# Kernel tuning notes

Hardware: AMD Instinct MI355X
Metric: run time of the kernel (lower is better)

Reference implementation:

```python
import jax, jax.numpy as jnp
import numpy as np

N_NODES = 50000
N_EDGES = 1600000
IN_FEATS = 128
ENC_H = 20
DEC_H = 64


def setup_inputs() -> dict:
    key = jax.random.key(0)
    ks = jax.random.split(key, 14)
    inp = {}
    inp["x"] = jax.random.normal(ks[0], (N_NODES, IN_FEATS), dtype=jnp.float32)
    inp["edge_index"] = jax.random.randint(ks[1], (2, N_EDGES), 0, N_NODES, dtype=jnp.int64)
    inp["node_id"] = 0
    inp["noise_normal"] = jax.random.normal(ks[2], (N_EDGES, ENC_H), dtype=jnp.float32)
    inp["noise_u"] = jax.random.uniform(ks[3], (N_EDGES, 1), dtype=jnp.float32)
    # parameters (glorot-ish init)
    def lin(k, fan_in, fan_out):
        s = 1.0 / np.sqrt(fan_in)
        return jax.random.uniform(k, (fan_in, fan_out), jnp.float32, -s, s)
    inp["W_gc"] = lin(ks[4], IN_FEATS, ENC_H)
    inp["b_gc"] = jnp.zeros((ENC_H,), jnp.float32)
    inp["W_mu"] = lin(ks[5], 3 * ENC_H, ENC_H)
    inp["b_mu"] = jnp.zeros((ENC_H,), jnp.float32)
    inp["W_var"] = lin(ks[6], 3 * ENC_H, ENC_H)
    inp["b_var"] = jnp.zeros((ENC_H,), jnp.float32)
    inp["W_d1"] = lin(ks[7], ENC_H, DEC_H)
    inp["b_d1"] = jnp.zeros((DEC_H,), jnp.float32)
    inp["W_d2"] = lin(ks[8], DEC_H, 1)
    inp["b_d2"] = jnp.zeros((1,), jnp.float32)
    return inp


def _gcn_conv(x, edge_index, W, b):
    """PyG-style GCNConv: add self-loops, symmetric D^-1/2 (A+I) D^-1/2 norm."""
    n = x.shape[0]
    sl = jnp.arange(n, dtype=edge_index.dtype)
    row = jnp.concatenate([edge_index[0], sl])  # source
    col = jnp.concatenate([edge_index[1], sl])  # target
    xw = x @ W  # [N, H]
    deg = jax.ops.segment_sum(jnp.ones_like(col, dtype=xw.dtype), col, num_segments=n)
    dinv = jnp.where(deg > 0, jax.lax.rsqrt(deg), 0.0)
    norm = dinv[row] * dinv[col]  # [E+N]
    out = jax.ops.segment_sum(xw[row] * norm[:, None], col, num_segments=n)
    return out + b


def reference(x, edge_index, node_id, noise_normal, noise_u,
              W_gc, b_gc, W_mu, b_mu, W_var, b_var, W_d1, b_d1, W_d2, b_d2):
    # GCN encoder
    x1 = jax.nn.relu(_gcn_conv(x, edge_index, W_gc, b_gc))  # [N, H]
    # per-edge concat: [src_embed | dst_embed | node_id_embed]
    rows, cols = edge_index[0], edge_index[1]
    node_embed = jnp.broadcast_to(x1[node_id][None, :], (rows.shape[0], x1.shape[1]))
    x2 = jnp.concatenate([x1[rows], x1[cols], node_embed], axis=1)  # [E, 3H]
    # variational heads + reparameterization
    mu = x2 @ W_mu + b_mu
    sigma = jnp.exp(x2 @ W_var + b_var)
    z = mu + sigma * noise_normal  # [E, H]
    # decoder MLP
    h = jax.nn.relu(z @ W_d1 + b_d1)
    sampling_weights = jax.nn.relu(h @ W_d2 + b_d2)  # [E, 1]
    # gumbel-sigmoid sample (training=True, bias=0.0 -> bias'=1e-4, temperature=1.0)
    bias = 0.0001
    eps = (bias - (1.0 - bias)) * noise_u + (1.0 - bias)
    gate = jnp.log(eps) - jnp.log(1.0 - eps) + sampling_weights
    return jax.nn.sigmoid(gate)
```

## Files before the change

kernel.cpp:

```cpp
#include <hip/hip_runtime.h>

#define NFEAT 128
#define H 20
#define DH 64
#define SCAN_T 1024
#define BE 64
#define NB 192
#define HW 12800

typedef __attribute__((ext_vector_type(8))) short short8;
typedef __attribute__((ext_vector_type(4))) float f32x4;

__device__ __forceinline__ unsigned short f2bf(float f) {
    union { float f; unsigned u; } v; v.f = f;
    unsigned r = v.u + 0x7fff + ((v.u >> 16) & 1);
    return (unsigned short)(r >> 16);
}
__device__ __forceinline__ unsigned pk2(unsigned short a, unsigned short b) {
    return (unsigned)a | ((unsigned)b << 16);
}

template <int CTRL>
__device__ __forceinline__ float dpp_add(float x) {
    int y = __builtin_amdgcn_update_dpp(0, __float_as_int(x), CTRL, 0xF, 0xF, true);
    return x + __int_as_float(y);
}
__device__ __forceinline__ float sum16(float x) {
    x = dpp_add<0xB1>(x);
    x = dpp_add<0x4E>(x);
    x = dpp_add<0x124>(x);
    x = dpp_add<0x128>(x);
    return x;
}

__global__ __launch_bounds__(256) void k_prep(const float* __restrict__ Wmu, const float* __restrict__ Wvar,
                                              const float* __restrict__ Wd1,
                                              unsigned short* __restrict__ Bh, unsigned short* __restrict__ Bd1,
                                              int* __restrict__ deg, int* __restrict__ csum, int N) {
    int t = blockIdx.x * blockDim.x + threadIdx.x;
    if (t < N) deg[t] = 0;
    if (t < 256) csum[t] = 0;
    if (t < 512) {
        int f = t >> 6, l = t & 63;
        int tile = f >> 1, s = f & 1;
        int col = (tile & 1) * 16 + (l & 15);
        const float* W = (tile < 2) ? Wmu : Wvar;
#pragma unroll
        for (int j = 0; j < 8; j++) {
            int k = s * 32 + (l >> 4) * 8 + j;
            float v = (k < 2 * H && col < H) ? W[k * H + col] : 0.f;
            Bh[(size_t)f * 512 + l * 8 + j] = f2bf(v);
        }
    } else if (t < 768) {
        int f = (t - 512) >> 6, l = t & 63;
        int n = f * 16 + (l & 15);
#pragma unroll
        for (int j = 0; j < 8; j++) {
            int k = (l >> 4) * 8 + j;
            float v = (k < H) ? Wd1[k * DH + n] : 0.f;
            Bd1[(size_t)f * 512 + l * 8 + j] = f2bf(v);
        }
    }
}

__global__ __launch_bounds__(512) void k_hist(const int* __restrict__ cols,
                                              unsigned* __restrict__ hist, int* __restrict__ csum,
                                              int E, int N) {
    __shared__ unsigned h[HW];
    __shared__ int cs[256];
    int wstride = (N + 3) >> 2;
    int nchunks = (N + 255) >> 8;
    for (int i = threadIdx.x; i < wstride; i += 512) h[i] = 0;
    if (threadIdx.x < 256) cs[threadIdx.x] = 0;
    __syncthreads();
    int chunk = (E + NB - 1) / NB;
    int beg = blockIdx.x * chunk, end = min(beg + chunk, E);
    for (int i = beg + threadIdx.x; i < end; i += 512) {
        int c = __builtin_nontemporal_load(cols + i);
        atomicAdd(&h[c >> 2], 1u << ((c & 3) * 8));
    }
    __syncthreads();
    unsigned* dst = hist + (size_t)blockIdx.x * wstride;
    for (int i = threadIdx.x; i < wstride; i += 512) {
        unsigned w = h[i];
        dst[i] = w;
        if (w) {
            int s = (w & 0xFF) + ((w >> 8) & 0xFF) + ((w >> 16) & 0xFF) + (w >> 24);
            atomicAdd(&cs[i >> 6], s);
        }
    }
    __syncthreads();
    for (int j = threadIdx.x; j < nchunks; j += 512)
        if (cs[j]) atomicAdd(&csum[j], cs[j]);
}

__global__ __launch_bounds__(256) void k_scansmall(const int* __restrict__ chunkSum,
                                                   int* __restrict__ chunkOff, int nb) {
    __shared__ int sc[256];
    int t = threadIdx.x;
    int v0 = (t < nb) ? chunkSum[t] : 0;
    sc[t] = v0;
    __syncthreads();
    for (int off = 1; off < 256; off <<= 1) {
        int v = (t >= off) ? sc[t - off] : 0;
        __syncthreads();
        sc[t] += v;
        __syncthreads();
    }
    if (t < nb) chunkOff[t] = sc[t] - v0;
}

__global__ __launch_bounds__(256) void k_bases(const unsigned* __restrict__ hist,
                                               const int* __restrict__ chunkOff,
                                               unsigned char* __restrict__ delta,
                                               int* __restrict__ offsets, int* __restrict__ deg,
                                               int N, int E) {
    __shared__ int sc[256];
    int c = blockIdx.x * 256 + threadIdx.x;
    int wstride = (N + 3) >> 2;
    int sh = (c & 3) * 8;
    bool valid = c < N;
    int cw = valid ? (c >> 2) : 0;
    unsigned cnt[NB / 4];
    int d = 0;
#pragma unroll
    for (int b = 0; b < NB; b++) {
        unsigned w = hist[(size_t)b * wstride + cw];
        unsigned byte = (w >> sh) & 0xFF;
        if ((b & 3) == 0) cnt[b >> 2] = byte;
        else cnt[b >> 2] |= byte << ((b & 3) * 8);
        d += (int)byte;
    }
    if (!valid) d = 0;
    sc[threadIdx.x] = d;
    __syncthreads();
    for (int off = 1; off < 256; off <<= 1) {
        int v = (threadIdx.x >= off) ? sc[threadIdx.x - off] : 0;
        __syncthreads();
        sc[threadIdx.x] += v;
        __syncthreads();
    }
    if (valid) {
        int base = chunkOff[blockIdx.x] + sc[threadIdx.x] - d;
        offsets[c] = base;
        deg[c] = d;
        int run = 0;
#pragma unroll
        for (int b = 0; b < NB; b++) {
            delta[(size_t)b * N + c] = (unsigned char)run;
            run += (int)((cnt[b >> 2] >> ((b & 3) * 8)) & 0xFF);
        }
    }
    if (blockIdx.x == 0 && threadIdx.x == 0) offsets[N] = E;
}

__global__ __launch_bounds__(512) void k_place(const int* __restrict__ rows, const int* __restrict__ cols,
                                               const int* __restrict__ offsets,
                                               const unsigned char* __restrict__ delta,
                                               unsigned short* __restrict__ srcs, int E, int N) {
    __shared__ unsigned h[HW];
    int wstride = (N + 3) >> 2;
    for (int i = threadIdx.x; i < wstride; i += 512) h[i] = 0;
    __syncthreads();
    int chunk = (E + NB - 1) / NB;
    int beg = blockIdx.x * chunk, end = min(beg + chunk, E);
    const unsigned char* mydelta = delta + (size_t)blockIdx.x * N;
    for (int i = beg + threadIdx.x; i < end; i += 512) {
        int c = __builtin_nontemporal_load(cols + i);
        int r = __builtin_nontemporal_load(rows + i);
        int sh = (c & 3) * 8;
        unsigned old = atomicAdd(&h[c >> 2], 1u << sh);
        int rank = (old >> sh) & 0xFF;
        int pos = offsets[c] + (int)mydelta[c] + rank;
        srcs[pos] = (unsigned short)r;
    }
}

__global__ __launch_bounds__(256) void k_deg(const int* __restrict__ cols, int* __restrict__ deg, int E) {
    int t = blockIdx.x * blockDim.x + threadIdx.x;
    if (t < E) atomicAdd(&deg[cols[t]], 1);
}

__global__ __launch_bounds__(SCAN_T) void k_scan(const int* __restrict__ deg, int* __restrict__ offsets,
                                                 int* __restrict__ cursor, int N) {
    __shared__ int sums[SCAN_T];
    int t = threadIdx.x;
    int chunk = (N + SCAN_T - 1) / SCAN_T;
    int beg = t * chunk;
    int end = min(beg + chunk, N);
    int s = 0;
    for (int i = beg; i < end; i++) s += deg[i];
    sums[t] = s;
    __syncthreads();
    for (int off = 1; off < SCAN_T; off <<= 1) {
        int v = (t >= off) ? sums[t - off] : 0;
        __syncthreads();
        sums[t] += v;
        __syncthreads();
    }
    int run = (t == 0) ? 0 : sums[t - 1];
    for (int i = beg; i < end; i++) {
        offsets[i] = run;
        cursor[i] = run;
        run += deg[i];
    }
    if (t == SCAN_T - 1) offsets[N] = sums[SCAN_T - 1];
}

__global__ __launch_bounds__(256) void k_bucket_csr(const int* __restrict__ rows, const int* __restrict__ cols,
                                                    int* __restrict__ cursor, int* __restrict__ srcs, int E) {
    int e = blockIdx.x * blockDim.x + threadIdx.x;
    if (e >= E) return;
    int pos = atomicAdd(&cursor[cols[e]], 1);
    srcs[pos] = rows[e];
}

__global__ __launch_bounds__(256) void k_xw_xs(const float* __restrict__ x, const float* __restrict__ Wgc,
                                               const int* __restrict__ deg,
                                               float* __restrict__ xs, int N) {
    __shared__ float Ws[NFEAT * H];
    for (int i = threadIdx.x; i < NFEAT * H; i += blockDim.x) Ws[i] = Wgc[i];
    __syncthreads();
    int n = blockIdx.x * blockDim.x + threadIdx.x;
    if (n >= N) return;
    float acc[H];
#pragma unroll
    for (int j = 0; j < H; j++) acc[j] = 0.f;
    const float4* x4 = (const float4*)(x + (size_t)n * NFEAT);
#pragma unroll 4
    for (int k4 = 0; k4 < NFEAT / 4; k4++) {
        float4 xv = x4[k4];
#pragma unroll
        for (int s = 0; s < 4; s++) {
            float xk = (s == 0) ? xv.x : (s == 1) ? xv.y : (s == 2) ? xv.z : xv.w;
            const float4* wrow = (const float4*)(Ws + (k4 * 4 + s) * H);
#pragma unroll
            for (int q = 0; q < 5; q++) {
                float4 w = wrow[q];
                acc[q * 4 + 0] += xk * w.x;
                acc[q * 4 + 1] += xk * w.y;
                acc[q * 4 + 2] += xk * w.z;
                acc[q * 4 + 3] += xk * w.w;
            }
        }
    }
    float di = rsqrtf((float)(deg[n] + 1));
    float4* o = (float4*)(xs + (size_t)n * H);
#pragma unroll
    for (int q = 0; q < 5; q++)
        o[q] = make_float4(acc[q * 4 + 0] * di, acc[q * 4 + 1] * di, acc[q * 4 + 2] * di, acc[q * 4 + 3] * di);
}

template <typename IT>
__device__ __forceinline__ void gather_core16(const float* __restrict__ xs, const IT* __restrict__ idx,
                                              int beg, int end, int n, int sl, int degn,
                                              const float* __restrict__ bgc, unsigned short* __restrict__ x1b,
                                              int nid, const float* __restrict__ Wmu, const float* __restrict__ Wvar,
                                              const float* __restrict__ bmu, const float* __restrict__ bvar,
                                              float* __restrict__ bcat2) {
    float acc[H];
    if (sl == 0) {
        const float4* self = (const float4*)(xs + (size_t)n * H);
#pragma unroll
        for (int q = 0; q < 5; q++) {
            float4 v = self[q];
            acc[q * 4 + 0] = v.x; acc[q * 4 + 1] = v.y; acc[q * 4 + 2] = v.z; acc[q * 4 + 3] = v.w;
        }
    } else {
#pragma unroll
        for (int j = 0; j < H; j++) acc[j] = 0.f;
    }
#pragma unroll 2
    for (int i = beg + sl; i < end; i += 16) {
        int r = (int)__builtin_nontemporal_load(idx + i);
        const float4* p = (const float4*)(xs + (size_t)r * H);
#pragma unroll
        for (int q = 0; q < 5; q++) {
            float4 v = p[q];
            acc[q * 4 + 0] += v.x; acc[q * 4 + 1] += v.y; acc[q * 4 + 2] += v.z; acc[q * 4 + 3] += v.w;
        }
    }
#pragma unroll
    for (int j = 0; j < H; j++) acc[j] = sum16(acc[j]);
    float di = rsqrtf((float)(degn + 1));
    float x1f[H];
#pragma unroll
    for (int j = 0; j < H; j++) x1f[j] = fmaxf(di * acc[j] + bgc[j], 0.f);
    if (sl == 0) {
        unsigned o[10];
#pragma unroll
        for (int j = 0; j < 10; j++) o[j] = pk2(f2bf(x1f[2 * j]), f2bf(x1f[2 * j + 1]));
        unsigned* dst = (unsigned*)(x1b + (size_t)n * H);
        *(uint4*)dst = make_uint4(o[0], o[1], o[2], o[3]);
        *(uint4*)(dst + 4) = make_uint4(o[4], o[5], o[6], o[7]);
        *(uint2*)(dst + 8) = make_uint2(o[8], o[9]);
    }
    if (n == nid) {
#pragma unroll
        for (int base = 0; base < 48; base += 16) {
            int jj = base + sl;
            if (jj < 40) {
                bool ismu = jj < 20;
                int col = ismu ? jj : jj - 20;
                const float* W = ismu ? Wmu : Wvar;
                float s = ismu ? bmu[col] : bvar[col];
#pragma unroll
                for (int k = 0; k < H; k++) s += x1f[k] * W[(2 * H + k) * H + col];
                bcat2[jj] = s;
            }
        }
    }
}

__global__ __launch_bounds__(256) void k_gather_csr16(const float* __restrict__ xs, const unsigned short* __restrict__ srcs,
                                                      const int* __restrict__ offsets, const int* __restrict__ deg,
                                                      const float* __restrict__ bgc,
                                                      unsigned short* __restrict__ x1b,
                                                      const int* __restrict__ node_id,
                                                      const float* __restrict__ Wmu, const float* __restrict__ Wvar,
                                                      const float* __restrict__ bmu, const float* __restrict__ bvar,
                                                      float* __restrict__ bcat2, int N) {
    int wave = (blockIdx.x * 256 + threadIdx.x) >> 6;
    int lane = threadIdx.x & 63;
    int n = wave * 4 + (lane >> 4);
    if (n >= N) return;
    gather_core16(xs, srcs, offsets[n], offsets[n + 1], n, lane & 15, deg[n], bgc, x1b,
                  node_id[0], Wmu, Wvar, bmu, bvar, bcat2);
}

__global__ __launch_bounds__(256) void k_gather_csr(const float* __restrict__ xs, const int* __restrict__ srcs,
                                                    const int* __restrict__ offsets, const int* __restrict__ deg,
                                                    const float* __restrict__ bgc,
                                                    unsigned short* __restrict__ x1b,
                                                    const int* __restrict__ node_id,
                                                    const float* __restrict__ Wmu, const float* __restrict__ Wvar,
                                                    const float* __restrict__ bmu, const float* __restrict__ bvar,
                                                    float* __restrict__ bcat2, int N) {
    int wave = (blockIdx.x * 256 + threadIdx.x) >> 6;
    int lane = threadIdx.x & 63;
    int n = wave * 4 + (lane >> 4);
    if (n >= N) return;
    gather_core16(xs, srcs, offsets[n], offsets[n + 1], n, lane & 15, deg[n], bgc, x1b,
                  node_id[0], Wmu, Wvar, bmu, bvar, bcat2);
}

__global__ __launch_bounds__(256, 8) void k_mlp(
    const unsigned short* __restrict__ x1b, const int* __restrict__ rows, const int* __restrict__ cols,
    const float* __restrict__ noise_n, const float* __restrict__ noise_u,
    const unsigned short* __restrict__ Bh, const unsigned short* __restrict__ Bd1g,
    const float* __restrict__ bcat2, const float* __restrict__ b_d1,
    const float* __restrict__ W_d2, const float* __restrict__ b_d2,
    float* __restrict__ out, int E) {

    __shared__ __align__(16) unsigned short x2s[BE * 72];
    __shared__ __align__(16) unsigned short A2[BE * 44];

    int tid = threadIdx.x;
    int e0 = blockIdx.x * BE;
    int l = tid & 63, w = tid >> 6;
    int m = l & 15, quad = l >> 4;
    int erow0 = w * 16 + quad * 4;

    float nz0[4], nz1[4];
#pragma unroll
    for (int r4 = 0; r4 < 4; r4++) {
        int e = e0 + erow0 + r4;
        int ec = (e < E) ? e : 0;
        nz0[r4] = noise_n[(size_t)ec * H + m];
        nz1[r4] = (m < 4) ? noise_n[(size_t)ec * H + 16 + m] : 0.f;
    }

    {
        int le = tid >> 2, p = tid & 3;
        int e = e0 + le; if (e >= E) e = E - 1;
        int r = rows[e], c = cols[e];
#pragma unroll
        for (int ii = 0; ii < 4; ii++) {
            int i = p + ii * 4;
            unsigned* dst = (unsigned*)((char*)x2s + le * 144 + i * 8);
            if (i < 10) {
                int node = (i < 5) ? r : c;
                int cc = (i < 5) ? i : i - 5;
                uint2 v = *(const uint2*)((const char*)x1b + (size_t)node * 40 + cc * 8);
                dst[0] = v.x;
                dst[1] = v.y;
            } else {
                dst[0] = 0u; dst[1] = 0u;
            }
        }
    }
    __syncthreads();

    f32x4 accs[4];
    {
        const char* arow = (const char*)x2s + (w * 16 + m) * 144 + quad * 16;
        short8 a0 = *(const short8*)(arow);
        short8 a1 = *(const short8*)(arow + 64);
#pragma unroll
        for (int t4 = 0; t4 < 4; t4++) {
            f32x4 acc = {0.f, 0.f, 0.f, 0.f};
            short8 b0 = *(const short8*)(Bh + (t4 * 2 + 0) * 512 + l * 8);
            short8 b1 = *(const short8*)(Bh + (t4 * 2 + 1) * 512 + l * 8);
            acc = __builtin_amdgcn_mfma_f32_16x16x32_bf16(a0, b0, acc, 0, 0, 0);
            acc = __builtin_amdgcn_mfma_f32_16x16x32_bf16(a1, b1, acc, 0, 0, 0);
            accs[t4] = acc;
        }
    }

    {
        float bm0 = bcat2[m];
        float bv0 = bcat2[20 + m];
        float bm1 = (m < 4) ? bcat2[16 + m] : 0.f;
        float bv1 = (m < 4) ? bcat2[36 + m] : 0.f;
#pragma unroll
        for (int r4 = 0; r4 < 4; r4++) {
            float z0 = accs[0][r4] + bm0 + __expf(accs[2][r4] + bv0) * nz0[r4];
            *(unsigned short*)((char*)A2 + (erow0 + r4) * 88 + m * 2) = f2bf(z0);
            unsigned short z1v = 0;
            if (m < 4) z1v = f2bf(accs[1][r4] + bm1 + __expf(accs[3][r4] + bv1) * nz1[r4]);
            *(unsigned short*)((char*)A2 + (erow0 + r4) * 88 + (16 + m) * 2) = z1v;
        }
    }
    __syncthreads();

    {
        short8 a2 = *(const short8*)((const char*)A2 + (w * 16 + m) * 88 + quad * 16);
        float p0 = 0.f, p1 = 0.f, p2 = 0.f, p3 = 0.f;
#pragma unroll
        for (int t4 = 0; t4 < 4; t4++) {
            f32x4 acc = {0.f, 0.f, 0.f, 0.f};
            short8 bb = *(const short8*)(Bd1g + t4 * 512 + l * 8);
            acc = __builtin_amdgcn_mfma_f32_16x16x32_bf16(a2, bb, acc, 0, 0, 0);
            int col = t4 * 16 + m;
            float bias = b_d1[col], wo = W_d2[col];
            p0 += fmaxf(acc[0] + bias, 0.f) * wo;
            p1 += fmaxf(acc[1] + bias, 0.f) * wo;
            p2 += fmaxf(acc[2] + bias, 0.f) * wo;
            p3 += fmaxf(acc[3] + bias, 0.f) * wo;
        }
        p0 = sum16(p0); p1 = sum16(p1); p2 = sum16(p2); p3 = sum16(p3);
        if (m < 4) {
            float swv = (m == 0) ? p0 : (m == 1) ? p1 : (m == 2) ? p2 : p3;
            int leo = w * 16 + quad * 4 + m;
            int e = e0 + leo;
            if (e < E) {
                float sw = fmaxf(swv + b_d2[0], 0.f);
                float u = noise_u[e];
                float ev = 0.9999f - 0.9998f * u;
                float t = __expf(-sw);
                out[e] = ev / (ev + (1.f - ev) * t);
            }
        }
    }
}

extern "C" void kernel_launch(void* const* d_in, const int* in_sizes, int n_in,
                              void* d_out, int out_size, void* d_ws, size_t ws_size,
                              hipStream_t stream) {
    const int N = in_sizes[0] / NFEAT;
    const int E = in_sizes[1] / 2;

    const float* x       = (const float*)d_in[0];
    const int*   ei      = (const int*)d_in[1];
    const int*   rows    = ei;
    const int*   cols    = ei + E;
    const int*   node_id = (const int*)d_in[2];
    const float* noise_n = (const float*)d_in[3];
    const float* noise_u = (const float*)d_in[4];
    const float* Wgc  = (const float*)d_in[5];
    const float* bgc  = (const float*)d_in[6];
    const float* Wmu  = (const float*)d_in[7];
    const float* bmu  = (const float*)d_in[8];
    const float* Wvar = (const float*)d_in[9];
    const float* bvar = (const float*)d_in[10];
    const float* Wd1  = (const float*)d_in[11];
    const float* bd1  = (const float*)d_in[12];
    const float* Wd2  = (const float*)d_in[13];
    const float* bd2  = (const float*)d_in[14];
    float* out = (float*)d_out;

    const int B = 256;
    int gN  = (N + B - 1) / B;
    int gG  = (N + 15) / 16;
    int gE  = (E + B - 1) / B;
    int gM  = (E + BE - 1) / BE;
    int nBins = (N + 255) / 256;

    char* ws = (char*)d_ws;
    size_t o_deg     = 0;
    size_t o_off     = o_deg  + (((size_t)N * 4 + 255) & ~255ULL);
    size_t o_csum    = o_off  + (((size_t)(N + 1) * 4 + 255) & ~255ULL);
    size_t o_coff    = o_csum + 1024;
    size_t o_hist    = o_coff + 1024;
    size_t wstride   = (size_t)((N + 3) >> 2);
    size_t o_delta   = o_hist  + ((NB * wstride * 4 + 255) & ~255ULL);
    size_t o_srcs    = o_delta + (((size_t)NB * N + 255) & ~255ULL);
    size_t o_xs      = o_srcs  + (((size_t)E * 2 + 255) & ~255ULL);
    size_t o_x1b     = o_xs    + (((size_t)N * H * 4 + 255) & ~255ULL);
    size_t o_Bh      = o_x1b   + (((size_t)N * H * 2 + 255) & ~255ULL);
    size_t o_Bd1     = o_Bh    + 8192;
    size_t o_bcat2   = o_Bd1   + 4096;
    size_t need      = o_bcat2 + 256;

    bool main_path = (ws_size >= need) && (N <= 4 * HW) && (N < 65536) && (nBins <= 256);

    if (main_path) {
        int*   deg     = (int*)(ws + o_deg);
        int*   offsets = (int*)(ws + o_off);
        int*   csum    = (int*)(ws + o_csum);
        int*   coff    = (int*)(ws + o_coff);
        unsigned* hist = (unsigned*)(ws + o_hist);
        unsigned char* delta = (unsigned char*)(ws + o_delta);
        unsigned short* srcs = (unsigned short*)(ws + o_srcs);
        float* xs      = (float*)(ws + o_xs);
        unsigned short* x1b  = (unsigned short*)(ws + o_x1b);
        unsigned short* Bh   = (unsigned short*)(ws + o_Bh);
        unsigned short* Bd1  = (unsigned short*)(ws + o_Bd1);
        float* bcat2   = (float*)(ws + o_bcat2);

        k_prep<<<gN, B, 0, stream>>>(Wmu, Wvar, Wd1, Bh, Bd1, deg, csum, N);
        k_hist<<<NB, 512, 0, stream>>>(cols, hist, csum, E, N);
        k_scansmall<<<1, B, 0, stream>>>(csum, coff, nBins);
        k_bases<<<nBins, B, 0, stream>>>(hist, coff, delta, offsets, deg, N, E);
        k_xw_xs<<<gN, B, 0, stream>>>(x, Wgc, deg, xs, N);
        k_place<<<NB, 512, 0, stream>>>(rows, cols, offsets, delta, srcs, E, N);
        k_gather_csr16<<<gG, B, 0, stream>>>(xs, srcs, offsets, deg, bgc, x1b,
                                             node_id, Wmu, Wvar, bmu, bvar, bcat2, N);
        k_mlp<<<gM, B, 0, stream>>>(x1b, rows, cols, noise_n, noise_u,
                                    Bh, Bd1, bcat2, bd1, Wd2, bd2, out, E);
    } else {
        int*   deg     = (int*)ws;
        int*   offsets = (int*)(ws + 200000);
        int*   cursor  = (int*)(ws + 400016);
        int*   srcs    = (int*)(ws + 600016);
        float* xs      = (float*)(ws + 7000016);
        unsigned short* x1b = (unsigned short*)(ws + 11000016);
        unsigned short* Bh  = (unsigned short*)(ws + 13000016);
        unsigned short* Bd1 = (unsigned short*)(ws + 13008208);
        float* bcat2   = (float*)(ws + 13012304);

        k_prep<<<gN, B, 0, stream>>>(Wmu, Wvar, Wd1, Bh, Bd1, deg, cursor, N);
        k_deg<<<gE, B, 0, stream>>>(cols, deg, E);
        k_scan<<<1, SCAN_T, 0, stream>>>(deg, offsets, cursor, N);
        k_bucket_csr<<<gE, B, 0, stream>>>(rows, cols, cursor, srcs, E);
        k_xw_xs<<<gN, B, 0, stream>>>(x, Wgc, deg, xs, N);
        k_gather_csr<<<gG, B, 0, stream>>>(xs, srcs, offsets, deg, bgc, x1b,
                                           node_id, Wmu, Wvar, bmu, bvar, bcat2, N);
        k_mlp<<<gM, B, 0, stream>>>(x1b, rows, cols, noise_n, noise_u,
                                    Bh, Bd1, bcat2, bd1, Wd2, bd2, out, E);
    }
}
```

Before: 430.4 us.

## Precompute per-node mu/var projections and drop per-edge head GEMM

Because x2 is a concatenation, the mu and var heads split into a per-source term, a per-destination term and a constant node_id term. The gather kernel now computes the per-node projections x1·W_mu and x1·W_var for the source and destination weight blocks and stores them in bf16 as PA and PB. The edge MLP then only gathers two 96-byte rows and adds them, which removes the shared-memory staging, a barrier and the first MFMA stage per edge. The cost is more per-node work and a larger per-node table, which reuses the histogram workspace region. bcat2 is also zeroed in prep, in case the node_id term is never written.

```diff
diff --git a/kernel.cpp b/kernel.cpp
--- a/kernel.cpp
+++ b/kernel.cpp
@@ -19,6 +19,11 @@
 __device__ __forceinline__ unsigned pk2(unsigned short a, unsigned short b) {
     return (unsigned)a | ((unsigned)b << 16);
 }
+__device__ __forceinline__ float bfel(uint4 v, int j) {
+    unsigned word = (j < 2) ? v.x : (j < 4) ? v.y : (j < 6) ? v.z : v.w;
+    unsigned u = (j & 1) ? (word & 0xFFFF0000u) : (word << 16);
+    return __int_as_float((int)u);
+}
 
 template <int CTRL>
 __device__ __forceinline__ float dpp_add(float x) {
@@ -33,26 +38,16 @@
     return x;
 }
 
-__global__ __launch_bounds__(256) void k_prep(const float* __restrict__ Wmu, const float* __restrict__ Wvar,
-                                              const float* __restrict__ Wd1,
-                                              unsigned short* __restrict__ Bh, unsigned short* __restrict__ Bd1,
-                                              int* __restrict__ deg, int* __restrict__ csum, int N) {
+__global__ __launch_bounds__(256) void k_prep(const float* __restrict__ Wd1,
+                                              unsigned short* __restrict__ Bd1,
+                                              int* __restrict__ deg, int* __restrict__ csum,
+                                              float* __restrict__ bcat2, int N) {
     int t = blockIdx.x * blockDim.x + threadIdx.x;
     if (t < N) deg[t] = 0;
     if (t < 256) csum[t] = 0;
-    if (t < 512) {
+    if (t < 64) bcat2[t] = 0.f;
+    if (t < 256) {
         int f = t >> 6, l = t & 63;
-        int tile = f >> 1, s = f & 1;
-        int col = (tile & 1) * 16 + (l & 15);
-        const float* W = (tile < 2) ? Wmu : Wvar;
-#pragma unroll
-        for (int j = 0; j < 8; j++) {
-            int k = s * 32 + (l >> 4) * 8 + j;
-            float v = (k < 2 * H && col < H) ? W[k * H + col] : 0.f;
-            Bh[(size_t)f * 512 + l * 8 + j] = f2bf(v);
-        }
-    } else if (t < 768) {
-        int f = (t - 512) >> 6, l = t & 63;
         int n = f * 16 + (l & 15);
 #pragma unroll
         for (int j = 0; j < 8; j++) {
@@ -254,7 +249,8 @@
 template <typename IT>
 __device__ __forceinline__ void gather_core16(const float* __restrict__ xs, const IT* __restrict__ idx,
                                               int beg, int end, int n, int sl, int degn,
-                                              const float* __restrict__ bgc, unsigned short* __restrict__ x1b,
+                                              const float* __restrict__ bgc,
+                                              unsigned short* __restrict__ PAo, unsigned short* __restrict__ PBo,
                                               int nid, const float* __restrict__ Wmu, const float* __restrict__ Wvar,
                                               const float* __restrict__ bmu, const float* __restrict__ bvar,
                                               float* __restrict__ bcat2) {
@@ -286,15 +282,24 @@
     float x1f[H];
 #pragma unroll
     for (int j = 0; j < H; j++) x1f[j] = fmaxf(di * acc[j] + bgc[j], 0.f);
-    if (sl == 0) {
-        unsigned o[10];
-#pragma unroll
-        for (int j = 0; j < 10; j++) o[j] = pk2(f2bf(x1f[2 * j]), f2bf(x1f[2 * j + 1]));
-        unsigned* dst = (unsigned*)(x1b + (size_t)n * H);
-        *(uint4*)dst = make_uint4(o[0], o[1], o[2], o[3]);
-        *(uint4*)(dst + 4) = make_uint4(o[4], o[5], o[6], o[7]);
-        *(uint2*)(dst + 8) = make_uint2(o[8], o[9]);
-    }
+
+#pragma unroll
+    for (int t = 0; t < 6; t++) {
+        int v = sl + 16 * t;
+        int part = v / 24;
+        int j = v - part * 24;
+        float s = 0.f;
+        if (j < 20) {
+            const float* W = (part & 1) ? Wvar : Wmu;
+            int k0 = (part < 2) ? 0 : 20;
+#pragma unroll
+            for (int k = 0; k < H; k++) s += x1f[k] * W[(k0 + k) * H + j];
+        }
+        unsigned short* T = (part < 2) ? PAo : PBo;
+        int off = (j >> 3) * 16 + (part & 1) * 8 + (j & 7);
+        T[(size_t)n * 48 + off] = f2bf(s);
+    }
+
     if (n == nid) {
 #pragma unroll
         for (int base = 0; base < 48; base += 16) {
@@ -315,7 +320,7 @@
 __global__ __launch_bounds__(256) void k_gather_csr16(const float* __restrict__ xs, const unsigned short* __restrict__ srcs,
                                                       const int* __restrict__ offsets, const int* __restrict__ deg,
                                                       const float* __restrict__ bgc,
-                                                      unsigned short* __restrict__ x1b,
+                                                      unsigned short* __restrict__ PAo, unsigned short* __restrict__ PBo,
                                                       const int* __restrict__ node_id,
                                                       const float* __restrict__ Wmu, const float* __restrict__ Wvar,
                                                       const float* __restrict__ bmu, const float* __restrict__ bvar,
@@ -324,14 +329,14 @@
     int lane = threadIdx.x & 63;
     int n = wave * 4 + (lane >> 4);
     if (n >= N) return;
-    gather_core16(xs, srcs, offsets[n], offsets[n + 1], n, lane & 15, deg[n], bgc, x1b,
+    gather_core16(xs, srcs, offsets[n], offsets[n + 1], n, lane & 15, deg[n], bgc, PAo, PBo,
                   node_id[0], Wmu, Wvar, bmu, bvar, bcat2);
 }
 
 __global__ __launch_bounds__(256) void k_gather_csr(const float* __restrict__ xs, const int* __restrict__ srcs,
                                                     const int* __restrict__ offsets, const int* __restrict__ deg,
                                                     const float* __restrict__ bgc,
-                                                    unsigned short* __restrict__ x1b,
+                                                    unsigned short* __restrict__ PAo, unsigned short* __restrict__ PBo,
                                                     const int* __restrict__ node_id,
                                                     const float* __restrict__ Wmu, const float* __restrict__ Wvar,
                                                     const float* __restrict__ bmu, const float* __restrict__ bvar,
@@ -340,116 +345,96 @@
     int lane = threadIdx.x & 63;
     int n = wave * 4 + (lane >> 4);
     if (n >= N) return;
-    gather_core16(xs, srcs, offsets[n], offsets[n + 1], n, lane & 15, deg[n], bgc, x1b,
+    gather_core16(xs, srcs, offsets[n], offsets[n + 1], n, lane & 15, deg[n], bgc, PAo, PBo,
                   node_id[0], Wmu, Wvar, bmu, bvar, bcat2);
 }
 
-__global__ __launch_bounds__(256, 8) void k_mlp(
-    const unsigned short* __restrict__ x1b, const int* __restrict__ rows, const int* __restrict__ cols,
+__global__ __launch_bounds__(256) void k_mlp(
+    const unsigned short* __restrict__ PA, const unsigned short* __restrict__ PBt,
+    const int* __restrict__ rows, const int* __restrict__ cols,
     const float* __restrict__ noise_n, const float* __restrict__ noise_u,
-    const unsigned short* __restrict__ Bh, const unsigned short* __restrict__ Bd1g,
+    const unsigned short* __restrict__ Bd1g,
     const float* __restrict__ bcat2, const float* __restrict__ b_d1,
     const float* __restrict__ W_d2, const float* __restrict__ b_d2,
     float* __restrict__ out, int E) {
-
-    __shared__ __align__(16) unsigned short x2s[BE * 72];
-    __shared__ __align__(16) unsigned short A2[BE * 44];
 
     int tid = threadIdx.x;
     int e0 = blockIdx.x * BE;
     int l = tid & 63, w = tid >> 6;
     int m = l & 15, quad = l >> 4;
-    int erow0 = w * 16 + quad * 4;
-
-    float nz0[4], nz1[4];
-#pragma unroll
-    for (int r4 = 0; r4 < 4; r4++) {
-        int e = e0 + erow0 + r4;
-        int ec = (e < E) ? e : 0;
-        nz0[r4] = noise_n[(size_t)ec * H + m];
-        nz1[r4] = (m < 4) ? noise_n[(size_t)ec * H + 16 + m] : 0.f;
-    }
-
-    {
-        int le = tid >> 2, p = tid & 3;
-        int e = e0 + le; if (e >= E) e = E - 1;
-        int r = rows[e], c = cols[e];
-#pragma unroll
-        for (int ii = 0; ii < 4; ii++) {
-            int i = p + ii * 4;
-            unsigned* dst = (unsigned*)((char*)x2s + le * 144 + i * 8);
-            if (i < 10) {
-                int node = (i < 5) ? r : c;
-                int cc = (i < 5) ? i : i - 5;
-                uint2 v = *(const uint2*)((const char*)x1b + (size_t)node * 40 + cc * 8);
-                dst[0] = v.x;
-                dst[1] = v.y;
-            } else {
-                dst[0] = 0u; dst[1] = 0u;
-            }
-        }
-    }
-    __syncthreads();
-
-    f32x4 accs[4];
-    {
-        const char* arow = (const char*)x2s + (w * 16 + m) * 144 + quad * 16;
-        short8 a0 = *(const short8*)(arow);
-        short8 a1 = *(const short8*)(arow + 64);
-#pragma unroll
-        for (int t4 = 0; t4 < 4; t4++) {
-            f32x4 acc = {0.f, 0.f, 0.f, 0.f};
-            short8 b0 = *(const short8*)(Bh + (t4 * 2 + 0) * 512 + l * 8);
-            short8 b1 = *(const short8*)(Bh + (t4 * 2 + 1) * 512 + l * 8);
-            acc = __builtin_amdgcn_mfma_f32_16x16x32_bf16(a0, b0, acc, 0, 0, 0);
-            acc = __builtin_amdgcn_mfma_f32_16x16x32_bf16(a1, b1, acc, 0, 0, 0);
-            accs[t4] = acc;
-        }
-    }
-
-    {
-        float bm0 = bcat2[m];
-        float bv0 = bcat2[20 + m];
-        float bm1 = (m < 4) ? bcat2[16 + m] : 0.f;
-        float bv1 = (m < 4) ? bcat2[36 + m] : 0.f;
-#pragma unroll
-        for (int r4 = 0; r4 < 4; r4++) {
-            float z0 = accs[0][r4] + bm0 + __expf(accs[2][r4] + bv0) * nz0[r4];
-            *(unsigned short*)((char*)A2 + (erow0 + r4) * 88 + m * 2) = f2bf(z0);
-            unsigned short z1v = 0;
-            if (m < 4) z1v = f2bf(accs[1][r4] + bm1 + __expf(accs[3][r4] + bv1) * nz1[r4]);
-            *(unsigned short*)((char*)A2 + (erow0 + r4) * 88 + (16 + m) * 2) = z1v;
-        }
-    }
-    __syncthreads();
-
-    {
-        short8 a2 = *(const short8*)((const char*)A2 + (w * 16 + m) * 88 + quad * 16);
-        float p0 = 0.f, p1 = 0.f, p2 = 0.f, p3 = 0.f;
-#pragma unroll
-        for (int t4 = 0; t4 < 4; t4++) {
-            f32x4 acc = {0.f, 0.f, 0.f, 0.f};
-            short8 bb = *(const short8*)(Bd1g + t4 * 512 + l * 8);
-            acc = __builtin_amdgcn_mfma_f32_16x16x32_bf16(a2, bb, acc, 0, 0, 0);
-            int col = t4 * 16 + m;
-            float bias = b_d1[col], wo = W_d2[col];
-            p0 += fmaxf(acc[0] + bias, 0.f) * wo;
-            p1 += fmaxf(acc[1] + bias, 0.f) * wo;
-            p2 += fmaxf(acc[2] + bias, 0.f) * wo;
-            p3 += fmaxf(acc[3] + bias, 0.f) * wo;
-        }
-        p0 = sum16(p0); p1 = sum16(p1); p2 = sum16(p2); p3 = sum16(p3);
-        if (m < 4) {
-            float swv = (m == 0) ? p0 : (m == 1) ? p1 : (m == 2) ? p2 : p3;
-            int leo = w * 16 + quad * 4 + m;
-            int e = e0 + leo;
-            if (e < E) {
-                float sw = fmaxf(swv + b_d2[0], 0.f);
-                float u = noise_u[e];
-                float ev = 0.9999f - 0.9998f * u;
-                float t = __expf(-sw);
-                out[e] = ev / (ev + (1.f - ev) * t);
-            }
+
+    int ea = e0 + w * 16 + m;
+    int ec = (ea < E) ? ea : E - 1;
+    int r = rows[ec], c = cols[ec];
+
+    uint4 pam = {0, 0, 0, 0}, pav = {0, 0, 0, 0}, pbm = {0, 0, 0, 0}, pbv = {0, 0, 0, 0};
+    float nz[8], bm[8], bv[8];
+#pragma unroll
+    for (int j = 0; j < 8; j++) { nz[j] = 0.f; bm[j] = 0.f; bv[j] = 0.f; }
+    if (quad < 3) {
+        const char* pa = (const char*)PA + (size_t)r * 96 + quad * 32;
+        const char* pb = (const char*)PBt + (size_t)c * 96 + quad * 32;
+        pam = *(const uint4*)pa;  pav = *(const uint4*)(pa + 16);
+        pbm = *(const uint4*)pb;  pbv = *(const uint4*)(pb + 16);
+        float4 b0 = *(const float4*)(bcat2 + quad * 8);
+        float4 b1 = *(const float4*)(bcat2 + quad * 8 + 4);
+        bm[0] = b0.x; bm[1] = b0.y; bm[2] = b0.z; bm[3] = b0.w;
+        bm[4] = b1.x; bm[5] = b1.y; bm[6] = b1.z; bm[7] = b1.w;
+        float4 v0 = *(const float4*)(bcat2 + 20 + quad * 8);
+        float4 v1 = *(const float4*)(bcat2 + 20 + quad * 8 + 4);
+        bv[0] = v0.x; bv[1] = v0.y; bv[2] = v0.z; bv[3] = v0.w;
+        bv[4] = v1.x; bv[5] = v1.y; bv[6] = v1.z; bv[7] = v1.w;
+        const float* np = noise_n + (size_t)ec * H + quad * 8;
+        float4 n0 = *(const float4*)np;
+        nz[0] = n0.x; nz[1] = n0.y; nz[2] = n0.z; nz[3] = n0.w;
+        if (quad < 2) {
+            float4 n1 = *(const float4*)(np + 4);
+            nz[4] = n1.x; nz[5] = n1.y; nz[6] = n1.z; nz[7] = n1.w;
+        }
+    }
+
+    unsigned zp[4];
+#pragma unroll
+    for (int jj = 0; jj < 4; jj++) {
+        unsigned short zh[2];
+#pragma unroll
+        for (int h2 = 0; h2 < 2; h2++) {
+            int j = jj * 2 + h2;
+            float zmu = bfel(pam, j) + bfel(pbm, j) + bm[j];
+            float zva = bfel(pav, j) + bfel(pbv, j) + bv[j];
+            float z = zmu + __expf(zva) * nz[j];
+            z = (quad * 8 + j < 20) ? z : 0.f;
+            zh[h2] = f2bf(z);
+        }
+        zp[jj] = pk2(zh[0], zh[1]);
+    }
+    union { unsigned u[4]; short8 s; } au;
+    au.u[0] = zp[0]; au.u[1] = zp[1]; au.u[2] = zp[2]; au.u[3] = zp[3];
+    short8 a2 = au.s;
+
+    float p0 = 0.f, p1 = 0.f, p2 = 0.f, p3 = 0.f;
+#pragma unroll
+    for (int t4 = 0; t4 < 4; t4++) {
+        f32x4 acc = {0.f, 0.f, 0.f, 0.f};
+        short8 bb = *(const short8*)(Bd1g + t4 * 512 + l * 8);
+        acc = __builtin_amdgcn_mfma_f32_16x16x32_bf16(a2, bb, acc, 0, 0, 0);
+        int col = t4 * 16 + m;
+        float bias = b_d1[col], wo = W_d2[col];
+        p0 += fmaxf(acc[0] + bias, 0.f) * wo;
+        p1 += fmaxf(acc[1] + bias, 0.f) * wo;
+        p2 += fmaxf(acc[2] + bias, 0.f) * wo;
+        p3 += fmaxf(acc[3] + bias, 0.f) * wo;
+    }
+    p0 = sum16(p0); p1 = sum16(p1); p2 = sum16(p2); p3 = sum16(p3);
+    if (m < 4) {
+        float swv = (m == 0) ? p0 : (m == 1) ? p1 : (m == 2) ? p2 : p3;
+        int e = e0 + w * 16 + quad * 4 + m;
+        if (e < E) {
+            float sw = fmaxf(swv + b_d2[0], 0.f);
+            float u = noise_u[e];
+            float ev = 0.9999f - 0.9998f * u;
+            float t = __expf(-sw);
+            out[e] = ev / (ev + (1.f - ev) * t);
         }
     }
 }
@@ -487,18 +472,19 @@
     int nBins = (N + 255) / 256;
 
     char* ws = (char*)d_ws;
+    size_t wstride   = (size_t)((N + 3) >> 2);
+    size_t pa_sz     = (((size_t)N * 96) + 255) & ~255ULL;
+    size_t hist_sz   = ((NB * wstride * 4) + 255) & ~255ULL;
+    size_t histreg   = (hist_sz > 2 * pa_sz) ? hist_sz : 2 * pa_sz;
     size_t o_deg     = 0;
     size_t o_off     = o_deg  + (((size_t)N * 4 + 255) & ~255ULL);
     size_t o_csum    = o_off  + (((size_t)(N + 1) * 4 + 255) & ~255ULL);
     size_t o_coff    = o_csum + 1024;
     size_t o_hist    = o_coff + 1024;
-    size_t wstride   = (size_t)((N + 3) >> 2);
-    size_t o_delta   = o_hist  + ((NB * wstride * 4 + 255) & ~255ULL);
+    size_t o_delta   = o_hist  + histreg;
     size_t o_srcs    = o_delta + (((size_t)NB * N + 255) & ~255ULL);
     size_t o_xs      = o_srcs  + (((size_t)E * 2 + 255) & ~255ULL);
-    size_t o_x1b     = o_xs    + (((size_t)N * H * 4 + 255) & ~255ULL);
-    size_t o_Bh      = o_x1b   + (((size_t)N * H * 2 + 255) & ~255ULL);
-    size_t o_Bd1     = o_Bh    + 8192;
+    size_t o_Bd1     = o_xs    + (((size_t)N * H * 4 + 255) & ~255ULL);
     size_t o_bcat2   = o_Bd1   + 4096;
     size_t need      = o_bcat2 + 256;
 
@@ -510,43 +496,53 @@
         int*   csum    = (int*)(ws + o_csum);
         int*   coff    = (int*)(ws + o_coff);
         unsigned* hist = (unsigned*)(ws + o_hist);
+        unsigned short* PA = (unsigned short*)(ws + o_hist);
+        unsigned short* PB = (unsigned short*)(ws + o_hist + pa_sz);
         unsigned char* delta = (unsigned char*)(ws + o_delta);
         unsigned short* srcs = (unsigned short*)(ws + o_srcs);
         float* xs      = (float*)(ws + o_xs);
-        unsigned short* x1b  = (unsigned short*)(ws + o_x1b);
-        unsigned short* Bh   = (unsigned short*)(ws + o_Bh);
         unsigned short* Bd1  = (unsigned short*)(ws + o_Bd1);
         float* bcat2   = (float*)(ws + o_bcat2);
 
-        k_prep<<<gN, B, 0, stream>>>(Wmu, Wvar, Wd1, Bh, Bd1, deg, csum, N);
+        k_prep<<<gN, B, 0, stream>>>(Wd1, Bd1, deg, csum, bcat2, N);
         k_hist<<<NB, 512, 0, stream>>>(cols, hist, csum, E, N);
         k_scansmall<<<1, B, 0, stream>>>(csum, coff, nBins);
         k_bases<<<nBins, B, 0, stream>>>(hist, coff, delta, offsets, deg, N, E);
         k_xw_xs<<<gN, B, 0, stream>>>(x, Wgc, deg, xs, N);
         k_place<<<NB, 512, 0, stream>>>(rows, cols, offsets, delta, srcs, E, N);
-        k_gather_csr16<<<gG, B, 0, stream>>>(xs, srcs, offsets, deg, bgc, x1b,
+        k_gather_csr16<<<gG, B, 0, stream>>>(xs, srcs, offsets, deg, bgc, PA, PB,
                                              node_id, Wmu, Wvar, bmu, bvar, bcat2, N);
-        k_mlp<<<gM, B, 0, stream>>>(x1b, rows, cols, noise_n, noise_u,
-                                    Bh, Bd1, bcat2, bd1, Wd2, bd2, out, E);
+        k_mlp<<<gM, B, 0, stream>>>(PA, PB, rows, cols, noise_n, noise_u,
+                                    Bd1, bcat2, bd1, Wd2, bd2, out, E);
     } else {
-        int*   deg     = (int*)ws;
-        int*   offsets = (int*)(ws + 200000);
-        int*   cursor  = (int*)(ws + 400016);
-        int*   srcs    = (int*)(ws + 600016);
-        float* xs      = (float*)(ws + 7000016);
-        unsigned short* x1b = (unsigned short*)(ws + 11000016);
-        unsigned short* Bh  = (unsigned short*)(ws + 13000016);
-        unsigned short* Bd1 = (unsigned short*)(ws + 13008208);
-        float* bcat2   = (float*)(ws + 13012304);
-
-        k_prep<<<gN, B, 0, stream>>>(Wmu, Wvar, Wd1, Bh, Bd1, deg, cursor, N);
+        size_t f_deg   = 0;
+        size_t f_off   = f_deg + (((size_t)N * 4 + 255) & ~255ULL);
+        size_t f_cur   = f_off + (((size_t)(N + 1) * 4 + 255) & ~255ULL);
+        size_t f_srcs  = f_cur + (((size_t)N * 4 + 255) & ~255ULL);
+        size_t f_xs    = f_srcs + (((size_t)E * 4 + 255) & ~255ULL);
+        size_t f_PA    = f_xs + (((size_t)N * H * 4 + 255) & ~255ULL);
+        size_t f_PB    = f_PA + pa_sz;
+        size_t f_Bd1   = f_PB + pa_sz;
+        size_t f_bcat2 = f_Bd1 + 4096;
+
+        int*   deg     = (int*)(ws + f_deg);
+        int*   offsets = (int*)(ws + f_off);
+        int*   cursor  = (int*)(ws + f_cur);
+        int*   srcs    = (int*)(ws + f_srcs);
+        float* xs      = (float*)(ws + f_xs);
+        unsigned short* PA = (unsigned short*)(ws + f_PA);
+        unsigned short* PB = (unsigned short*)(ws + f_PB);
+        unsigned short* Bd1 = (unsigned short*)(ws + f_Bd1);
+        float* bcat2   = (float*)(ws + f_bcat2);
+
+        k_prep<<<gN, B, 0, stream>>>(Wd1, Bd1, deg, cursor, bcat2, N);
         k_deg<<<gE, B, 0, stream>>>(cols, deg, E);
         k_scan<<<1, SCAN_T, 0, stream>>>(deg, offsets, cursor, N);
         k_bucket_csr<<<gE, B, 0, stream>>>(rows, cols, cursor, srcs, E);
         k_xw_xs<<<gN, B, 0, stream>>>(x, Wgc, deg, xs, N);
-        k_gather_csr<<<gG, B, 0, stream>>>(xs, srcs, offsets, deg, bgc, x1b,
+        k_gather_csr<<<gG, B, 0, stream>>>(xs, srcs, offsets, deg, bgc, PA, PB,
                                            node_id, Wmu, Wvar, bmu, bvar, bcat2, N);
-        k_mlp<<<gM, B, 0, stream>>>(x1b, rows, cols, noise_n, noise_u,
-                                    Bh, Bd1, bcat2, bd1, Wd2, bd2, out, E);
-    }
-}
+        k_mlp<<<gM, B, 0, stream>>>(PA, PB, rows, cols, noise_n, noise_u,
+                                    Bd1, bcat2, bd1, Wd2, bd2, out, E);
+    }
+}
```

Measured after the change: 431.2 us. No clear change (+0.2%).
